# Kernel tuning notes

Measured on AMD Instinct MI355X. Metric: run time of the kernel, lower is better.

The kernel has to match this reference:

```python
import jax, jax.numpy as jnp
import numpy as np

K = 16  # num neighbors


def setup_inputs() -> dict:
    key = jax.random.key(0)
    ks = jax.random.split(key, 10)
    B, N, d_in, d_out = 4, 8192, 64, 128
    h = d_out // 2
    return {
        "xyz": jax.random.normal(ks[0], (B, 3, N), jnp.float32),
        "feature": jax.random.normal(ks[1], (B, d_in, N), jnp.float32),
        "w1": jax.random.normal(ks[2], (h, 10), jnp.float32) * 0.1,
        "b1": jax.random.normal(ks[3], (h,), jnp.float32) * 0.1,
        "w2": jax.random.normal(ks[4], (h, h), jnp.float32) * 0.1,
        "b2": jax.random.normal(ks[5], (h,), jnp.float32) * 0.1,
        "w3": jax.random.normal(ks[6], (h, h), jnp.float32) * 0.1,
        "b3": jax.random.normal(ks[7], (h,), jnp.float32) * 0.1,
        "ws": jax.random.normal(ks[8], (d_out, d_in), jnp.float32) * 0.1,
        "bs": jax.random.normal(ks[9], (d_out,), jnp.float32) * 0.1,
    }


def reference(xyz, feature, w1, b1, w2, b2, w3, b3, ws, bs):
    # xyz: [B,3,N], feature: [B,d_in,N]
    xyz_t = jnp.transpose(xyz, (0, 2, 1))  # [B,N,3]
    sq = jnp.sum(xyz_t * xyz_t, axis=-1)  # [B,N]
    # squared pairwise distance [B,N,N]
    dist = sq[:, :, None] + sq[:, None, :] - 2.0 * jnp.einsum("bnc,bmc->bnm", xyz_t, xyz_t)
    _, idx = jax.lax.top_k(-dist, K)  # smallest-k -> [B,N,K]
    # gather neighbor coords: [B,N,K,3]
    knn_xyz = jax.vmap(lambda pts, ind: pts[ind])(xyz_t, idx)
    center = jnp.broadcast_to(xyz_t[:, :, None, :], knn_xyz.shape)  # [B,N,K,3]
    diff = knn_xyz - center
    dsq = jnp.sum(diff * diff, axis=-1, keepdims=True)  # [B,N,K,1]
    pos = jnp.concatenate([center, knn_xyz, diff, dsq], axis=-1)  # [B,N,K,10]
    # three 1x1 convs over channel dim (no activations, faithful to source)
    h = jnp.einsum("bnkc,oc->bnko", pos, w1) + b1
    h = jnp.einsum("bnkc,oc->bnko", h, w2) + b2
    h = jnp.einsum("bnkc,oc->bnko", h, w3) + b3
    fe = jnp.max(h, axis=2)  # max-pool over neighbors -> [B,N,d_out//2]
    fe = jnp.transpose(fe, (0, 2, 1))  # [B,d_out//2,N]
    shortcut = jnp.einsum("bcn,oc->bon", feature, ws) + bs[None, :, None]
    return jnp.concatenate([fe, fe], axis=1) + shortcut  # [B,d_out,N]
```

## Files before the change

kernel.cpp:

```cpp
#include <hip/hip_runtime.h>

#define B_ 4
#define N_ 8192
#define DIN 64
#define HDIM 64
#define DOUT 128
#define KNN 16
#define QPB 64
#define PART 8
#define NTHR (QPB * PART)
#define CHUNK (N_ / PART)
#define CAP 16
#define CAPP 17
#define BLOCKS_PER_B (N_ / QPB)
#define GMARGIN 1e-3f

__global__ __launch_bounds__(256) void k_prep(
    const float* __restrict__ xyz,
    const float* __restrict__ w1, const float* __restrict__ b1,
    const float* __restrict__ w2, const float* __restrict__ b2,
    const float* __restrict__ w3, const float* __restrict__ b3,
    float4* __restrict__ pk, float4* __restrict__ prm) {
  const int blk = blockIdx.x, t = threadIdx.x;
  const int b = blk >> 5;
  const int m = ((blk & 31) << 8) + t;
  const float* xb = xyz + (size_t)b * 3 * N_;
  float x = xb[m], y = xb[N_ + m], z = xb[2 * N_ + m];
  float sq = __fadd_rn(__fadd_rn(__fmul_rn(x, x), __fmul_rn(y, y)), __fmul_rn(z, z));
  pk[((size_t)b << 13) + m] = make_float4(x, y, z, sq);

  if (blk == 0) {
    __shared__ float M2[HDIM][10];
    __shared__ float bb[HDIM];
    const int o = t;
    if (o < HDIM) {
      float r[10];
#pragma unroll
      for (int c = 0; c < 10; c++) r[c] = 0.f;
      float s = b2[o];
      for (int l = 0; l < HDIM; l++) {
        float w = w2[o * HDIM + l];
#pragma unroll
        for (int c = 0; c < 10; c++) r[c] = fmaf(w, w1[l * 10 + c], r[c]);
        s = fmaf(w, b1[l], s);
      }
#pragma unroll
      for (int c = 0; c < 10; c++) M2[o][c] = r[c];
      bb[o] = s;
    }
    __syncthreads();
    if (o < HDIM) {
      float r3[10];
#pragma unroll
      for (int c = 0; c < 10; c++) r3[c] = 0.f;
      float bc = b3[o];
      for (int l = 0; l < HDIM; l++) {
        float w = w3[o * HDIM + l];
#pragma unroll
        for (int c = 0; c < 10; c++) r3[c] = fmaf(w, M2[l][c], r3[c]);
        bc = fmaf(w, bb[l], bc);
      }
      prm[o]      = make_float4(r3[0] - r3[6], r3[1] - r3[7], r3[2] - r3[8], bc);
      prm[64 + o] = make_float4(r3[3] + r3[6], r3[4] + r3[7], r3[5] + r3[8], r3[9]);
    }
  }
}

#define MAX16(VARR, VMAX)                                                     \
  {                                                                           \
    float _m0 = fmaxf(fmaxf(VARR[0], VARR[1]), VARR[2]);                      \
    float _m1 = fmaxf(fmaxf(VARR[3], VARR[4]), VARR[5]);                      \
    float _m2 = fmaxf(fmaxf(VARR[6], VARR[7]), VARR[8]);                      \
    float _m3 = fmaxf(fmaxf(VARR[9], VARR[10]), VARR[11]);                    \
    float _m4 = fmaxf(fmaxf(VARR[12], VARR[13]), VARR[14]);                   \
    float _a = fmaxf(fmaxf(_m0, _m1), _m2);                                   \
    float _b = fmaxf(fmaxf(_m3, _m4), VARR[15]);                              \
    VMAX = fmaxf(_a, _b);                                                     \
  }

#define INSERT16(VARR, IARR, VMAX, DVAL, MIDX)                    \
  {                                                               \
    bool done = false;                                            \
    _Pragma("unroll") for (int _i = 0; _i < KNN; _i++) {          \
      bool hit = (!done) && (VARR[_i] == VMAX);                   \
      if (hit) { VARR[_i] = (DVAL); IARR[_i] = (MIDX); }          \
      done = done | hit;                                          \
    }                                                             \
    MAX16(VARR, VMAX);                                            \
  }

#define FLUSH()                                                               \
  {                                                                           \
    _Pragma("unroll") for (int c0_ = 0; c0_ < CAP; c0_ += 8) {                \
      int mi_[8]; float4 fc_[8];                                              \
      _Pragma("unroll") for (int e_ = 0; e_ < 8; e_++)                        \
        mi_[e_] = poolI[lbase + c0_ + e_] & (N_ - 1);                         \
      _Pragma("unroll") for (int e_ = 0; e_ < 8; e_++)                        \
        fc_[e_] = pk[bb + mi_[e_]];                                           \
      _Pragma("unroll") for (int e_ = 0; e_ < 8; e_++) {                      \
        if (c0_ + e_ < cnt) {                                                 \
          float dot_ = fmaf(fc_[e_].z, qz,                                    \
                       fmaf(fc_[e_].y, qy, __fmul_rn(fc_[e_].x, qx)));        \
          float d_ = fmaf(-2.0f, dot_, __fadd_rn(qs, fc_[e_].w));             \
          if (d_ < vmax) { INSERT16(v, id, vmax, d_, mi_[e_]); }              \
        }                                                                     \
      }                                                                       \
    }                                                                         \
    cnt = 0;                                                                  \
    unsigned old_ = atomicMin(&tau[q], __float_as_uint(vmax));                \
    gate = fminf(vmax, __uint_as_float(old_));                                \
    G = __fadd_rn(__fsub_rn(gate, qs), GMARGIN);                              \
  }

#define PROC8(CARR, U0)                                                       \
  {                                                                           \
    if (__any(cnt > CAP - 8)) { FLUSH(); }                                    \
    _Pragma("unroll") for (int e = 0; e < 8; e++) {                           \
      float gg = fmaf(CARR[e].x, nx2, fmaf(CARR[e].y, ny2,                    \
                  fmaf(CARR[e].z, nz2, CARR[e].w)));                          \
      if (gg < G) {                                                           \
        poolI[lbase + cnt] = (unsigned short)(jC + (U0) + e);                 \
        cnt++;                                                                \
      }                                                                       \
    }                                                                         \
  }

__global__ __launch_bounds__(NTHR, 4) void k_knn_fe(
    const float4* __restrict__ pk, const float4* __restrict__ prm,
    const float* __restrict__ feature, const float* __restrict__ wsM,
    const float* __restrict__ bs, float* __restrict__ out) {
  const int blk = blockIdx.x;
  const int b  = blk / BLOCKS_PER_B;
  const int n0 = (blk % BLOCKS_PER_B) * QPB;
  const int t = threadIdx.x;
  const int q = t & 63;
  const int j = __builtin_amdgcn_readfirstlane(t >> 6);
  const int lbase = t * CAPP;
  const size_t bb = (size_t)b << 13;

  __shared__ unsigned tau[QPB];
  __shared__ float4 prmL[2 * HDIM];
  __shared__ alignas(16) float poolF[128 * QPB];
  __shared__ alignas(16) unsigned short poolI[CAPP * NTHR];

  if (t < QPB) tau[t] = 0x7f800000u;
  for (int i = t; i < 2 * HDIM; i += NTHR) prmL[i] = prm[i];

  const float4 qv = pk[bb + n0 + q];
  const float qx = qv.x, qy = qv.y, qz = qv.z, qs = qv.w;
  const float nx2 = -2.0f * qx, ny2 = -2.0f * qy, nz2 = -2.0f * qz;

  const float INF = __uint_as_float(0x7f800000u);
  float v[KNN]; int id[KNN];
  float vmax, gate, G;
  int cnt = 0;
  __syncthreads();

  const float4* pj = pk + bb + (size_t)j * CHUNK;
  const int jC = j * CHUNK;

  {
    float4 c[KNN];
#pragma unroll
    for (int e = 0; e < KNN; e++) c[e] = pj[e];
#pragma unroll
    for (int e = 0; e < KNN; e++) {
      float dot = fmaf(c[e].z, qz, fmaf(c[e].y, qy, __fmul_rn(c[e].x, qx)));
      v[e] = fmaf(-2.0f, dot, __fadd_rn(qs, c[e].w));
      id[e] = jC + e;
    }
    MAX16(v, vmax);
    unsigned old = atomicMin(&tau[q], __float_as_uint(vmax));
    gate = fminf(vmax, __uint_as_float(old));
    G = __fadd_rn(__fsub_rn(gate, qs), GMARGIN);
  }

  {
    float4 ca[8], cb[8];
#pragma unroll
    for (int e = 0; e < 8; e++) ca[e] = pj[KNN + e];
    for (int u0 = KNN; u0 < CHUNK; u0 += 16) {
#pragma unroll
      for (int e = 0; e < 8; e++) cb[e] = pj[u0 + 8 + e];
      PROC8(ca, u0);
#pragma unroll
      for (int e = 0; e < 8; e++) ca[e] = pj[u0 + 16 + e];
      PROC8(cb, u0 + 8);
    }
  }
  FLUSH();
  __syncthreads();

#pragma unroll
  for (int i = 0; i < KNN; i++) {
    poolF[(j * KNN + i) * QPB + q] = v[i];
    poolI[(j * KNN + i) * QPB + q] = (unsigned short)id[i];
  }
  __syncthreads();

  float fv[KNN]; int fid[KNN]; float fm = INF;
  if (j < 4) {
    const int l0 = (2 * j) * KNN, r1 = (2 * j + 1) * KNN;
#pragma unroll
    for (int i = 0; i < KNN; i++) {
      fv[i] = poolF[(l0 + i) * QPB + q];
      fid[i] = poolI[(l0 + i) * QPB + q];
    }
    MAX16(fv, fm);
    for (int s = 0; s < KNN; s++) {
      float d = poolF[(r1 + s) * QPB + q];
      if (d < fm) { int m_ = poolI[(r1 + s) * QPB + q]; INSERT16(fv, fid, fm, d, m_); }
    }
#pragma unroll
    for (int i = 0; i < KNN; i++) {
      poolF[(l0 + i) * QPB + q] = fv[i];
      poolI[(l0 + i) * QPB + q] = (unsigned short)fid[i];
    }
  }
  __syncthreads();
  if (j < 2) {
    const int l0 = (4 * j) * KNN, r1 = (4 * j + 2) * KNN;
#pragma unroll
    for (int i = 0; i < KNN; i++) {
      fv[i] = poolF[(l0 + i) * QPB + q];
      fid[i] = poolI[(l0 + i) * QPB + q];
    }
    MAX16(fv, fm);
    for (int s = 0; s < KNN; s++) {
      float d = poolF[(r1 + s) * QPB + q];
      if (d < fm) { int m_ = poolI[(r1 + s) * QPB + q]; INSERT16(fv, fid, fm, d, m_); }
    }
#pragma unroll
    for (int i = 0; i < KNN; i++) {
      poolF[(l0 + i) * QPB + q] = fv[i];
      poolI[(l0 + i) * QPB + q] = (unsigned short)fid[i];
    }
  }
  __syncthreads();
  if (j == 0) {
#pragma unroll
    for (int i = 0; i < KNN; i++) {
      fv[i] = poolF[i * QPB + q];
      fid[i] = poolI[i * QPB + q];
    }
    MAX16(fv, fm);
    for (int s = 0; s < KNN; s++) {
      float d = poolF[(4 * KNN + s) * QPB + q];
      if (d < fm) { int m_ = poolI[(4 * KNN + s) * QPB + q]; INSERT16(fv, fid, fm, d, m_); }
    }
#pragma unroll
    for (int i = 0; i < KNN; i++) poolI[i * QPB + q] = (unsigned short)fid[i];
  }
  __syncthreads();

#pragma unroll
  for (int kk = 0; kk < 2; kk++) {
    int k = j * 2 + kk;
    int m = poolI[k * QPB + q];
    float4 c = pk[bb + m];
    float dx = __fsub_rn(c.x, qx), dy = __fsub_rn(c.y, qy), dz = __fsub_rn(c.z, qz);
    float dsq = __fadd_rn(__fadd_rn(__fmul_rn(dx, dx), __fmul_rn(dy, dy)),
                          __fmul_rn(dz, dz));
    poolF[k * QPB + q] = c.x;
    poolF[(KNN + k) * QPB + q] = c.y;
    poolF[(2 * KNN + k) * QPB + q] = c.z;
    poolF[(3 * KNN + k) * QPB + q] = dsq;
  }
  __syncthreads();

  float fo[8];
  {
    float nx[KNN], ny[KNN], nz[KNN], nd[KNN];
#pragma unroll
    for (int k = 0; k < KNN; k++) {
      nx[k] = poolF[k * QPB + q];
      ny[k] = poolF[(KNN + k) * QPB + q];
      nz[k] = poolF[(2 * KNN + k) * QPB + q];
      nd[k] = poolF[(3 * KNN + k) * QPB + q];
    }
#pragma unroll
    for (int oi = 0; oi < 8; oi++) {
      int o = j * 8 + oi;
      float4 pA = prmL[o], pB = prmL[HDIM + o];
      float basev = fmaf(qz, pA.z, fmaf(qy, pA.y, fmaf(qx, pA.x, pA.w)));
      float mx = -INF;
#pragma unroll
      for (int k = 0; k < KNN; k++) {
        float tv = fmaf(nz[k], pB.z,
                   fmaf(ny[k], pB.y,
                   fmaf(nx[k], pB.x, __fmul_rn(nd[k], pB.w))));
        mx = fmaxf(mx, tv);
      }
      fo[oi] = basev + mx;
    }
  }
  __syncthreads();

  float* wsL = poolF;
  float* feL = (float*)poolI;
  for (int i = t; i < DOUT * DIN; i += NTHR) wsL[i] = wsM[i];
#pragma unroll
  for (int r = 0; r < 8; r++) {
    int c = j * 8 + r;
    feL[c * QPB + q] = feature[(size_t)(b * DIN + c) * N_ + n0 + q];
  }
  __syncthreads();

  float acc[16];
#pragma unroll
  for (int oi = 0; oi < 16; oi++) acc[oi] = 0.f;
  for (int c4 = 0; c4 < DIN / 4; c4++) {
    float f0 = feL[(4 * c4 + 0) * QPB + q];
    float f1 = feL[(4 * c4 + 1) * QPB + q];
    float f2 = feL[(4 * c4 + 2) * QPB + q];
    float f3 = feL[(4 * c4 + 3) * QPB + q];
#pragma unroll
    for (int oi = 0; oi < 16; oi++) {
      int o = (oi < 8) ? (j * 8 + oi) : (64 + j * 8 + oi - 8);
      float4 w = ((const float4*)(wsL + o * DIN))[c4];
      acc[oi] = fmaf(w.x, f0, acc[oi]);
      acc[oi] = fmaf(w.y, f1, acc[oi]);
      acc[oi] = fmaf(w.z, f2, acc[oi]);
      acc[oi] = fmaf(w.w, f3, acc[oi]);
    }
  }
  float* ob = out + (size_t)b * DOUT * N_ + n0 + q;
#pragma unroll
  for (int oi = 0; oi < 16; oi++) {
    int o = (oi < 8) ? (j * 8 + oi) : (64 + j * 8 + oi - 8);
    ob[(size_t)o * N_] = acc[oi] + bs[o] + fo[oi & 7];
  }
}

extern "C" void kernel_launch(void* const* d_in, const int* in_sizes, int n_in,
                              void* d_out, int out_size, void* d_ws, size_t ws_size,
                              hipStream_t stream) {
  const float* xyz     = (const float*)d_in[0];
  const float* feature = (const float*)d_in[1];
  const float* w1 = (const float*)d_in[2];
  const float* b1 = (const float*)d_in[3];
  const float* w2 = (const float*)d_in[4];
  const float* b2 = (const float*)d_in[5];
  const float* w3 = (const float*)d_in[6];
  const float* b3 = (const float*)d_in[7];
  const float* wsM = (const float*)d_in[8];
  const float* bs  = (const float*)d_in[9];
  float* out = (float*)d_out;

  float4* prm = (float4*)d_ws;
  float4* pkB = (float4*)((char*)d_ws + 8192);

  hipLaunchKernelGGL(k_prep, dim3(128), dim3(256), 0, stream,
                     xyz, w1, b1, w2, b2, w3, b3, pkB, prm);
  hipLaunchKernelGGL(k_knn_fe, dim3(B_ * BLOCKS_PER_B), dim3(NTHR), 0, stream,
                     pkB, prm, feature, wsM, bs, out);
}
```

Baseline: 263.3 us.

## Split KNN search into separate kernel with two blocks per query tile

The fused knn+feature kernel is split into a k_knn kernel that launches twice as many blocks, each scanning half the candidate points. It writes partial top-16 lists (indices and distances) into the output buffer as scratch, and a separate k_fe kernel merges the two halves and then does the position MLP and shortcut. The scan filter now computes the exact distance instead of a margin-adjusted gate, and the shared threshold is polled each iteration to tighten the gate sooner. This raises occupancy and parallelism for the dominant search phase, at the cost of an extra launch and global round-trips through the output buffer.

```diff
diff --git a/kernel.cpp b/kernel.cpp
--- a/kernel.cpp
+++ b/kernel.cpp
@@ -9,11 +9,10 @@
 #define QPB 64
 #define PART 8
 #define NTHR (QPB * PART)
-#define CHUNK (N_ / PART)
+#define CHUNK2 512
 #define CAP 16
 #define CAPP 17
 #define BLOCKS_PER_B (N_ / QPB)
-#define GMARGIN 1e-3f
 
 __global__ __launch_bounds__(256) void k_prep(
     const float* __restrict__ xyz,
@@ -94,7 +93,7 @@
     _Pragma("unroll") for (int c0_ = 0; c0_ < CAP; c0_ += 8) {                \
       int mi_[8]; float4 fc_[8];                                              \
       _Pragma("unroll") for (int e_ = 0; e_ < 8; e_++)                        \
-        mi_[e_] = poolI[lbase + c0_ + e_] & (N_ - 1);                         \
+        mi_[e_] = scanI[lbase + c0_ + e_] & (N_ - 1);                         \
       _Pragma("unroll") for (int e_ = 0; e_ < 8; e_++)                        \
         fc_[e_] = pk[bb + mi_[e_]];                                           \
       _Pragma("unroll") for (int e_ = 0; e_ < 8; e_++) {                      \
@@ -109,23 +108,150 @@
     cnt = 0;                                                                  \
     unsigned old_ = atomicMin(&tau[q], __float_as_uint(vmax));                \
     gate = fminf(vmax, __uint_as_float(old_));                                \
-    G = __fadd_rn(__fsub_rn(gate, qs), GMARGIN);                              \
   }
 
 #define PROC8(CARR, U0)                                                       \
   {                                                                           \
     if (__any(cnt > CAP - 8)) { FLUSH(); }                                    \
+    gate = fminf(gate, __uint_as_float(tnext));                               \
+    tnext = tau[q];                                                           \
     _Pragma("unroll") for (int e = 0; e < 8; e++) {                           \
-      float gg = fmaf(CARR[e].x, nx2, fmaf(CARR[e].y, ny2,                    \
-                  fmaf(CARR[e].z, nz2, CARR[e].w)));                          \
-      if (gg < G) {                                                           \
-        poolI[lbase + cnt] = (unsigned short)(jC + (U0) + e);                 \
+      float dot_ = fmaf(CARR[e].z, qz,                                        \
+                   fmaf(CARR[e].y, qy, __fmul_rn(CARR[e].x, qx)));            \
+      float d_ = fmaf(-2.0f, dot_, __fadd_rn(qs, CARR[e].w));                 \
+      if (d_ < gate) {                                                        \
+        scanI[lbase + cnt] = (unsigned short)(base + (U0) + e);               \
         cnt++;                                                                \
       }                                                                       \
     }                                                                         \
   }
 
-__global__ __launch_bounds__(NTHR, 4) void k_knn_fe(
+__global__ __launch_bounds__(NTHR, 8) void k_knn(
+    const float4* __restrict__ pk, float* __restrict__ out) {
+  const int blk = blockIdx.x;
+  const int b   = blk >> 8;
+  const int rem = blk & 255;
+  const int n0  = (rem >> 1) * QPB;
+  const int h   = rem & 1;
+  const int t = threadIdx.x;
+  const int q = t & 63;
+  const int j = __builtin_amdgcn_readfirstlane(t >> 6);
+  const int lbase = t * CAPP;
+  const size_t bb = (size_t)b << 13;
+
+  __shared__ unsigned tau[QPB];
+  __shared__ alignas(16) unsigned char poolRaw[24576];
+  unsigned short* scanI = (unsigned short*)poolRaw;
+  float* Xd = (float*)poolRaw;
+  unsigned short* Xi = (unsigned short*)(poolRaw + 16384);
+
+  if (t < QPB) tau[t] = 0x7f800000u;
+
+  const float4 qv = pk[bb + n0 + q];
+  const float qx = qv.x, qy = qv.y, qz = qv.z, qs = qv.w;
+
+  float v[KNN]; int id[KNN];
+  float vmax, gate;
+  int cnt = 0;
+  __syncthreads();
+
+  const int base = h * (PART * CHUNK2) + j * CHUNK2;
+  const float4* pj = pk + bb + base;
+
+  {
+    float4 c[KNN];
+#pragma unroll
+    for (int e = 0; e < KNN; e++) c[e] = pj[e];
+#pragma unroll
+    for (int e = 0; e < KNN; e++) {
+      float dot = fmaf(c[e].z, qz, fmaf(c[e].y, qy, __fmul_rn(c[e].x, qx)));
+      v[e] = fmaf(-2.0f, dot, __fadd_rn(qs, c[e].w));
+      id[e] = base + e;
+    }
+    MAX16(v, vmax);
+    unsigned old = atomicMin(&tau[q], __float_as_uint(vmax));
+    gate = fminf(vmax, __uint_as_float(old));
+  }
+
+  {
+    unsigned tnext = tau[q];
+    float4 ca[8], cb[8];
+#pragma unroll
+    for (int e = 0; e < 8; e++) ca[e] = pj[KNN + e];
+    for (int u0 = KNN; u0 < CHUNK2; u0 += 16) {
+#pragma unroll
+      for (int e = 0; e < 8; e++) cb[e] = pj[u0 + 8 + e];
+      PROC8(ca, u0);
+      int pf = (u0 + 16 < CHUNK2) ? u0 + 16 : 0;
+#pragma unroll
+      for (int e = 0; e < 8; e++) ca[e] = pj[pf + e];
+      PROC8(cb, u0 + 8);
+    }
+  }
+  FLUSH();
+  __syncthreads();
+
+  float fv[KNN]; int fid[KNN]; float fm = vmax;
+#pragma unroll
+  for (int i = 0; i < KNN; i++) { fv[i] = v[i]; fid[i] = id[i]; }
+
+  if (j & 1) {
+    const int s = j >> 1;
+#pragma unroll
+    for (int i = 0; i < KNN; i++) {
+      Xd[(s * KNN + i) * QPB + q] = fv[i];
+      Xi[(s * KNN + i) * QPB + q] = (unsigned short)fid[i];
+    }
+  }
+  __syncthreads();
+  if (!(j & 1)) {
+    const int s = j >> 1;
+    for (int ss = 0; ss < KNN; ss++) {
+      float d = Xd[(s * KNN + ss) * QPB + q];
+      if (d < fm) { int m_ = Xi[(s * KNN + ss) * QPB + q]; INSERT16(fv, fid, fm, d, m_); }
+    }
+  }
+  __syncthreads();
+  if (j == 2 || j == 6) {
+    const int s = j >> 2;
+#pragma unroll
+    for (int i = 0; i < KNN; i++) {
+      Xd[(s * KNN + i) * QPB + q] = fv[i];
+      Xi[(s * KNN + i) * QPB + q] = (unsigned short)fid[i];
+    }
+  }
+  __syncthreads();
+  if (j == 0 || j == 4) {
+    const int s = j >> 2;
+    for (int ss = 0; ss < KNN; ss++) {
+      float d = Xd[(s * KNN + ss) * QPB + q];
+      if (d < fm) { int m_ = Xi[(s * KNN + ss) * QPB + q]; INSERT16(fv, fid, fm, d, m_); }
+    }
+  }
+  __syncthreads();
+  if (j == 4) {
+#pragma unroll
+    for (int i = 0; i < KNN; i++) {
+      Xd[i * QPB + q] = fv[i];
+      Xi[i * QPB + q] = (unsigned short)fid[i];
+    }
+  }
+  __syncthreads();
+  if (j == 0) {
+    for (int ss = 0; ss < KNN; ss++) {
+      float d = Xd[ss * QPB + q];
+      if (d < fm) { int m_ = Xi[ss * QPB + q]; INSERT16(fv, fid, fm, d, m_); }
+    }
+    float* ob = out + (size_t)b * DOUT * N_ + n0 + q;
+#pragma unroll
+    for (int i = 0; i < KNN; i++) {
+      ob[(size_t)(h * 32 + i) * N_]       = __uint_as_float((unsigned)fid[i]);
+      ob[(size_t)(h * 32 + KNN + i) * N_] = fv[i];
+    }
+  }
+}
+
+__global__ __launch_bounds__(NTHR, 2) void k_fe(
     const float4* __restrict__ pk, const float4* __restrict__ prm,
     const float* __restrict__ feature, const float* __restrict__ wsM,
     const float* __restrict__ bs, float* __restrict__ out) {
@@ -135,136 +261,55 @@
   const int t = threadIdx.x;
   const int q = t & 63;
   const int j = __builtin_amdgcn_readfirstlane(t >> 6);
-  const int lbase = t * CAPP;
   const size_t bb = (size_t)b << 13;
-
-  __shared__ unsigned tau[QPB];
+  const float INF = __uint_as_float(0x7f800000u);
+
   __shared__ float4 prmL[2 * HDIM];
-  __shared__ alignas(16) float poolF[128 * QPB];
-  __shared__ alignas(16) unsigned short poolI[CAPP * NTHR];
-
-  if (t < QPB) tau[t] = 0x7f800000u;
+  __shared__ float gp[4 * KNN * QPB];
+  __shared__ float feL[DIN * QPB];
+  __shared__ alignas(16) float wsL[DOUT * DIN];
+
   for (int i = t; i < 2 * HDIM; i += NTHR) prmL[i] = prm[i];
+  for (int i = t; i < DOUT * DIN / 4; i += NTHR)
+    ((float4*)wsL)[i] = ((const float4*)wsM)[i];
+#pragma unroll
+  for (int r = 0; r < 8; r++) {
+    int c = j * 8 + r;
+    feL[c * QPB + q] = feature[(size_t)(b * DIN + c) * N_ + n0 + q];
+  }
 
   const float4 qv = pk[bb + n0 + q];
-  const float qx = qv.x, qy = qv.y, qz = qv.z, qs = qv.w;
-  const float nx2 = -2.0f * qx, ny2 = -2.0f * qy, nz2 = -2.0f * qz;
-
-  const float INF = __uint_as_float(0x7f800000u);
-  float v[KNN]; int id[KNN];
-  float vmax, gate, G;
-  int cnt = 0;
-  __syncthreads();
-
-  const float4* pj = pk + bb + (size_t)j * CHUNK;
-  const int jC = j * CHUNK;
-
-  {
-    float4 c[KNN];
-#pragma unroll
-    for (int e = 0; e < KNN; e++) c[e] = pj[e];
-#pragma unroll
-    for (int e = 0; e < KNN; e++) {
-      float dot = fmaf(c[e].z, qz, fmaf(c[e].y, qy, __fmul_rn(c[e].x, qx)));
-      v[e] = fmaf(-2.0f, dot, __fadd_rn(qs, c[e].w));
-      id[e] = jC + e;
-    }
-    MAX16(v, vmax);
-    unsigned old = atomicMin(&tau[q], __float_as_uint(vmax));
-    gate = fminf(vmax, __uint_as_float(old));
-    G = __fadd_rn(__fsub_rn(gate, qs), GMARGIN);
-  }
-
-  {
-    float4 ca[8], cb[8];
-#pragma unroll
-    for (int e = 0; e < 8; e++) ca[e] = pj[KNN + e];
-    for (int u0 = KNN; u0 < CHUNK; u0 += 16) {
-#pragma unroll
-      for (int e = 0; e < 8; e++) cb[e] = pj[u0 + 8 + e];
-      PROC8(ca, u0);
-#pragma unroll
-      for (int e = 0; e < 8; e++) ca[e] = pj[u0 + 16 + e];
-      PROC8(cb, u0 + 8);
-    }
-  }
-  FLUSH();
-  __syncthreads();
-
+  const float qx = qv.x, qy = qv.y, qz = qv.z;
+
+  float* ob = out + (size_t)b * DOUT * N_ + n0 + q;
+
+  float fv[KNN]; int fid[KNN]; float fm;
 #pragma unroll
   for (int i = 0; i < KNN; i++) {
-    poolF[(j * KNN + i) * QPB + q] = v[i];
-    poolI[(j * KNN + i) * QPB + q] = (unsigned short)id[i];
-  }
-  __syncthreads();
-
-  float fv[KNN]; int fid[KNN]; float fm = INF;
-  if (j < 4) {
-    const int l0 = (2 * j) * KNN, r1 = (2 * j + 1) * KNN;
-#pragma unroll
-    for (int i = 0; i < KNN; i++) {
-      fv[i] = poolF[(l0 + i) * QPB + q];
-      fid[i] = poolI[(l0 + i) * QPB + q];
-    }
-    MAX16(fv, fm);
-    for (int s = 0; s < KNN; s++) {
-      float d = poolF[(r1 + s) * QPB + q];
-      if (d < fm) { int m_ = poolI[(r1 + s) * QPB + q]; INSERT16(fv, fid, fm, d, m_); }
-    }
-#pragma unroll
-    for (int i = 0; i < KNN; i++) {
-      poolF[(l0 + i) * QPB + q] = fv[i];
-      poolI[(l0 + i) * QPB + q] = (unsigned short)fid[i];
-    }
-  }
-  __syncthreads();
-  if (j < 2) {
-    const int l0 = (4 * j) * KNN, r1 = (4 * j + 2) * KNN;
-#pragma unroll
-    for (int i = 0; i < KNN; i++) {
-      fv[i] = poolF[(l0 + i) * QPB + q];
-      fid[i] = poolI[(l0 + i) * QPB + q];
-    }
-    MAX16(fv, fm);
-    for (int s = 0; s < KNN; s++) {
-      float d = poolF[(r1 + s) * QPB + q];
-      if (d < fm) { int m_ = poolI[(r1 + s) * QPB + q]; INSERT16(fv, fid, fm, d, m_); }
-    }
-#pragma unroll
-    for (int i = 0; i < KNN; i++) {
-      poolF[(l0 + i) * QPB + q] = fv[i];
-      poolI[(l0 + i) * QPB + q] = (unsigned short)fid[i];
-    }
-  }
-  __syncthreads();
-  if (j == 0) {
-#pragma unroll
-    for (int i = 0; i < KNN; i++) {
-      fv[i] = poolF[i * QPB + q];
-      fid[i] = poolI[i * QPB + q];
-    }
-    MAX16(fv, fm);
-    for (int s = 0; s < KNN; s++) {
-      float d = poolF[(4 * KNN + s) * QPB + q];
-      if (d < fm) { int m_ = poolI[(4 * KNN + s) * QPB + q]; INSERT16(fv, fid, fm, d, m_); }
-    }
-#pragma unroll
-    for (int i = 0; i < KNN; i++) poolI[i * QPB + q] = (unsigned short)fid[i];
-  }
-  __syncthreads();
+    fid[i] = (int)(__float_as_uint(ob[(size_t)i * N_]) & (N_ - 1));
+    fv[i]  = ob[(size_t)(KNN + i) * N_];
+  }
+  MAX16(fv, fm);
+  for (int s = 0; s < KNN; s++) {
+    float d = ob[(size_t)(48 + s) * N_];
+    if (d < fm) {
+      int m_ = (int)(__float_as_uint(ob[(size_t)(32 + s) * N_]) & (N_ - 1));
+      INSERT16(fv, fid, fm, d, m_);
+    }
+  }
 
 #pragma unroll
   for (int kk = 0; kk < 2; kk++) {
     int k = j * 2 + kk;
-    int m = poolI[k * QPB + q];
+    int m = fid[k];
     float4 c = pk[bb + m];
     float dx = __fsub_rn(c.x, qx), dy = __fsub_rn(c.y, qy), dz = __fsub_rn(c.z, qz);
     float dsq = __fadd_rn(__fadd_rn(__fmul_rn(dx, dx), __fmul_rn(dy, dy)),
                           __fmul_rn(dz, dz));
-    poolF[k * QPB + q] = c.x;
-    poolF[(KNN + k) * QPB + q] = c.y;
-    poolF[(2 * KNN + k) * QPB + q] = c.z;
-    poolF[(3 * KNN + k) * QPB + q] = dsq;
+    gp[k * QPB + q] = c.x;
+    gp[(KNN + k) * QPB + q] = c.y;
+    gp[(2 * KNN + k) * QPB + q] = c.z;
+    gp[(3 * KNN + k) * QPB + q] = dsq;
   }
   __syncthreads();
 
@@ -273,10 +318,10 @@
     float nx[KNN], ny[KNN], nz[KNN], nd[KNN];
 #pragma unroll
     for (int k = 0; k < KNN; k++) {
-      nx[k] = poolF[k * QPB + q];
-      ny[k] = poolF[(KNN + k) * QPB + q];
-      nz[k] = poolF[(2 * KNN + k) * QPB + q];
-      nd[k] = poolF[(3 * KNN + k) * QPB + q];
+      nx[k] = gp[k * QPB + q];
+      ny[k] = gp[(KNN + k) * QPB + q];
+      nz[k] = gp[(2 * KNN + k) * QPB + q];
+      nd[k] = gp[(3 * KNN + k) * QPB + q];
     }
 #pragma unroll
     for (int oi = 0; oi < 8; oi++) {
@@ -294,17 +339,6 @@
       fo[oi] = basev + mx;
     }
   }
-  __syncthreads();
-
-  float* wsL = poolF;
-  float* feL = (float*)poolI;
-  for (int i = t; i < DOUT * DIN; i += NTHR) wsL[i] = wsM[i];
-#pragma unroll
-  for (int r = 0; r < 8; r++) {
-    int c = j * 8 + r;
-    feL[c * QPB + q] = feature[(size_t)(b * DIN + c) * N_ + n0 + q];
-  }
-  __syncthreads();
 
   float acc[16];
 #pragma unroll
@@ -324,7 +358,6 @@
       acc[oi] = fmaf(w.w, f3, acc[oi]);
     }
   }
-  float* ob = out + (size_t)b * DOUT * N_ + n0 + q;
 #pragma unroll
   for (int oi = 0; oi < 16; oi++) {
     int o = (oi < 8) ? (j * 8 + oi) : (64 + j * 8 + oi - 8);
@@ -352,6 +385,8 @@
 
   hipLaunchKernelGGL(k_prep, dim3(128), dim3(256), 0, stream,
                      xyz, w1, b1, w2, b2, w3, b3, pkB, prm);
-  hipLaunchKernelGGL(k_knn_fe, dim3(B_ * BLOCKS_PER_B), dim3(NTHR), 0, stream,
+  hipLaunchKernelGGL(k_knn, dim3(B_ * 256), dim3(NTHR), 0, stream,
+                     pkB, out);
+  hipLaunchKernelGGL(k_fe, dim3(B_ * BLOCKS_PER_B), dim3(NTHR), 0, stream,
                      pkB, prm, feature, wsM, bs, out);
 }
```

Result: slower. 636.2 us (+141.6%).
